# Kernel tuning notes

Measured on AMD Instinct MI355X. Metric: run time of the kernel, lower is better.

Reference implementation:

```python
import jax, jax.numpy as jnp
import numpy as np
from functools import partial

V, E, H, F = 32000, 256, 512, 256  # vocab, embed_dim, hidden_dim, num_filters
FS = (3, 4, 5)

def setup_inputs() -> dict:
    key = jax.random.key(0)
    ks = jax.random.split(key, 24)
    s = 0.02
    d = {}
    d["src"] = jax.random.randint(ks[0], (32, 512), 0, V)
    d["trg"] = jax.random.randint(ks[1], (32, 64), 0, V)
    # embeddings with padding_idx=0 zeroed
    d["enc_emb"] = (jax.random.normal(ks[2], (V, E)) * s).at[0].set(0.0)
    d["dec_emb"] = (jax.random.normal(ks[3], (V, E)) * s).at[0].set(0.0)
    # conv1d weights (out_channels=F, in_channels=E, kernel)
    d["conv_w3"] = jax.random.normal(ks[4], (F, E, 3)) * s
    d["conv_b3"] = jnp.zeros((F,))
    d["conv_w4"] = jax.random.normal(ks[5], (F, E, 4)) * s
    d["conv_b4"] = jnp.zeros((F,))
    d["conv_w5"] = jax.random.normal(ks[6], (F, E, 5)) * s
    d["conv_b5"] = jnp.zeros((F,))
    d["fc1_w"] = jax.random.normal(ks[7], (H, 3 * F)) * s
    d["fc1_b"] = jnp.zeros((H,))
    d["fc2_w"] = jax.random.normal(ks[8], (H, H)) * s
    d["fc2_b"] = jnp.zeros((H,))
    # 2-layer LSTM: layer1 input E+H, layer2 input H; gates order i,f,g,o
    d["w_ih1"] = jax.random.normal(ks[9], (4 * H, E + H)) * s
    d["w_hh1"] = jax.random.normal(ks[10], (4 * H, H)) * s
    d["b_ih1"] = jnp.zeros((4 * H,))
    d["b_hh1"] = jnp.zeros((4 * H,))
    d["w_ih2"] = jax.random.normal(ks[11], (4 * H, H)) * s
    d["w_hh2"] = jax.random.normal(ks[12], (4 * H, H)) * s
    d["b_ih2"] = jnp.zeros((4 * H,))
    d["b_hh2"] = jnp.zeros((4 * H,))
    d["out_w"] = jax.random.normal(ks[13], (V, H)) * s
    d["out_b"] = jnp.zeros((V,))
    return d

def _lstm_cell(x, h, c, w_ih, w_hh, b_ih, b_hh):
    gates = x @ w_ih.T + b_ih + h @ w_hh.T + b_hh  # (B, 4H)
    i, f, g, o = jnp.split(gates, 4, axis=-1)
    c_new = jax.nn.sigmoid(f) * c + jax.nn.sigmoid(i) * jnp.tanh(g)
    h_new = jax.nn.sigmoid(o) * jnp.tanh(c_new)
    return h_new, c_new

def _encoder(src, enc_emb, convs, fc1_w, fc1_b, fc2_w, fc2_b):
    x = enc_emb[src]                    # (B, S, E)
    x = jnp.transpose(x, (0, 2, 1))     # (B, E, S)
    pooled = []
    for w, b in convs:
        y = jax.lax.conv_general_dilated(
            x, w, window_strides=(1,), padding='VALID',
            dimension_numbers=('NCH', 'OIH', 'NCH'))  # (B, F, S-k+1)
        pooled.append(jnp.max(jax.nn.relu(y + b[None, :, None]), axis=2))
    cat = jnp.concatenate(pooled, axis=1)              # (B, 3F)
    h = jax.nn.relu(cat @ fc1_w.T + fc1_b)             # (B, H)
    return h @ fc2_w.T + fc2_b                         # (B, H)

def reference(src, trg, enc_emb, conv_w3, conv_b3, conv_w4, conv_b4,
              conv_w5, conv_b5, fc1_w, fc1_b, fc2_w, fc2_b, dec_emb,
              w_ih1, w_hh1, b_ih1, b_hh1, w_ih2, w_hh2, b_ih2, b_hh2,
              out_w, out_b):
    B, T = trg.shape
    enc_out = _encoder(src, enc_emb,
                       [(conv_w3, conv_b3), (conv_w4, conv_b4), (conv_w5, conv_b5)],
                       fc1_w, fc1_b, fc2_w, fc2_b)  # (B, H)

    def step(carry, tok):
        h1, c1, h2, c2 = carry
        x = jnp.concatenate([dec_emb[tok], enc_out], axis=1)  # (B, E+H)
        h1, c1 = _lstm_cell(x, h1, c1, w_ih1, w_hh1, b_ih1, b_hh1)
        h2, c2 = _lstm_cell(h1, h2, c2, w_ih2, w_hh2, b_ih2, b_hh2)
        logits = h2 @ out_w.T + out_b                          # (B, V)
        return (h1, c1, h2, c2), logits

    z = jnp.zeros((B, H), dtype=enc_out.dtype)
    tokens = trg[:, :-1].T  # teacher forcing (ratio=1.0): (T-1, B)
    _, logits = jax.lax.scan(step, (z, z, z, z), tokens)       # (T-1, B, V)
    logits = jnp.transpose(logits, (1, 0, 2))                  # (B, T-1, V)
    # outputs[:, 0] is left as zeros, matching the torch loop starting at t=1
    return jnp.concatenate([jnp.zeros((B, 1, logits.shape[-1]), logits.dtype), logits], axis=1)
```

## Files before the change

### kernel.cpp

```cpp
#include <hip/hip_runtime.h>
#include <math.h>
#include <stdint.h>

#define B_    32
#define E_    256
#define F_    256
#define H_    512
#define V_    32000
#define G4    2048

typedef unsigned short u16;
typedef unsigned long long u64;
typedef __attribute__((ext_vector_type(8))) short bf16x8;
typedef __attribute__((ext_vector_type(4))) float f32x4;

__device__ __forceinline__ float fsig(float x) {
  return __builtin_amdgcn_rcpf(1.f + __expf(-x));
}
__device__ __forceinline__ float ftanh(float x) {
  return 1.f - 2.f * __builtin_amdgcn_rcpf(1.f + __expf(2.f * x));
}

__device__ __forceinline__ u16 f2bf(float f) {
  uint32_t u = __float_as_uint(f);
  uint32_t r = (u + 0x7FFFu + ((u >> 16) & 1u)) >> 16;
  return (u16)r;
}
__device__ __forceinline__ uint32_t pack2(float a, float b) {
  return (uint32_t)f2bf(a) | ((uint32_t)f2bf(b) << 16);
}

#define GLOAD16(gp, lp) __builtin_amdgcn_global_load_lds( \
    (const __attribute__((address_space(1))) uint32_t*)(const void*)(gp), \
    (__attribute__((address_space(3))) uint32_t*)(void*)(lp), 16, 0, 0)

#define ALOAD(P) __hip_atomic_load((P), __ATOMIC_RELAXED, __HIP_MEMORY_SCOPE_AGENT)
#define ASTORE(P, V) __hip_atomic_store((P), (V), __ATOMIC_RELAXED, __HIP_MEMORY_SCOPE_AGENT)

__global__ void init_all(float* pooled, uint32_t* sent1, uint32_t* sent2,
                         u16* h1d, u16* h2a,
                         const float* bi1, const float* bh1,
                         const float* bi2, const float* bh2,
                         float* bs1, float* bs2, float* out) {
  int i = blockIdx.x * blockDim.x + threadIdx.x, st = gridDim.x * blockDim.x;
  for (int k = i; k < 24576; k += st) pooled[k] = 0.f;
  for (int k = i; k < 131072; k += st) {
    uint32_t v = (k < 2048 && (k & 15) == 0) ? 1u : 0u;
    sent1[k] = v; sent2[k] = v;
  }
  uint4 z = {0u, 0u, 0u, 0u};
  for (int k = i; k < 2048; k += st) { ((uint4*)h1d)[k] = z; ((uint4*)h2a)[k] = z; }
  for (int k = i; k < G4; k += st) { bs1[k] = bi1[k] + bh1[k]; bs2[k] = bi2[k] + bh2[k]; }
  for (int k = i; k < B_ * V_; k += st) {
    int b = k / V_, v = k - b * V_;
    out[(size_t)b * 64 * V_ + v] = 0.f;
  }
}

__global__ void cvt_all(const float* s0, u16* d0, const float* s1, u16* d1,
                        const float* s2, u16* d2, const float* s3, u16* d3,
                        const float* s4, u16* d4) {
  int i = blockIdx.x * blockDim.x + threadIdx.x, st = gridDim.x * blockDim.x;
  for (; i < 2637824; i += st) {
    int j = i; const float* s; u16* d;
    if (j < 2048000) { s = s0; d = d0; }
    else if ((j -= 2048000) < 196608) { s = s1; d = d1; }
    else if ((j -= 196608) < 131072) { s = s2; d = d2; }
    else if ((j -= 131072) < 131072) { s = s3; d = d3; }
    else { j -= 131072; s = s4; d = d4; }
    const float4* sp = (const float4*)s + 2 * (size_t)j;
    float4 a = sp[0], b = sp[1];
    uint4 u;
    u.x = pack2(a.x, a.y); u.y = pack2(a.z, a.w);
    u.z = pack2(b.x, b.y); u.w = pack2(b.z, b.w);
    *((uint4*)d + j) = u;
  }
}

__global__ void wtj_all(const float* w3, u16* t3, const float* w4, u16* t4,
                        const float* w5, u16* t5) {
  int i = blockIdx.x * blockDim.x + threadIdx.x, st = gridDim.x * blockDim.x;
  for (; i < 786432; i += st) {
    int j = i; const float* w; u16* wt; int kw;
    if (j < 196608) { w = w3; wt = t3; kw = 3; }
    else if ((j -= 196608) < 262144) { w = w4; wt = t4; kw = 4; }
    else { j -= 262144; w = w5; wt = t5; kw = 5; }
    int f = j / (kw * 256);
    int r = j - f * (kw * 256);
    int jj = r >> 8, e = r & 255;
    wt[j] = f2bf(w[(f * 256 + e) * kw + jj]);
  }
}

__global__ void build_x1(const int* __restrict__ trg, const float* __restrict__ demb,
                         const float* __restrict__ enco, u16* __restrict__ X1) {
  int r = blockIdx.x, tid = threadIdx.x;
  u16* row = X1 + (size_t)r * 768;
  if (r >= 2016) { row[tid] = 0; row[256 + tid] = 0; row[512 + tid] = 0; return; }
  int t = r >> 5, b = r & 31;
  int tok = trg[b * 64 + t];
  row[tid]       = f2bf(demb[(size_t)tok * E_ + tid]);
  row[256 + tid] = f2bf(enco[b * H_ + tid]);
  row[512 + tid] = f2bf(enco[b * H_ + 256 + tid]);
}

__global__ void gemm_small(const float* __restrict__ A, const float* __restrict__ W,
                           const float* __restrict__ bias, float* __restrict__ C,
                           int K, int N, int relu) {
  int nl = threadIdx.x & 7, b = threadIdx.x >> 3;
  int n = blockIdx.x * 8 + nl;
  const float* a = A + b * K;
  const float* w = W + (size_t)n * K;
  float acc = 0.f;
  for (int k = 0; k < K; k += 4) {
    float4 av = *reinterpret_cast<const float4*>(&a[k]);
    float4 wv = *reinterpret_cast<const float4*>(&w[k]);
    acc = fmaf(av.x, wv.x, acc); acc = fmaf(av.y, wv.y, acc);
    acc = fmaf(av.z, wv.z, acc); acc = fmaf(av.w, wv.w, acc);
  }
  acc += bias[n];
  if (relu) acc = fmaxf(acc, 0.f);
  C[b * N + n] = acc;
}

__global__ __launch_bounds__(256)
void gemm_mfma(const u16* __restrict__ A, const u16* __restrict__ Bw,
               const float* __restrict__ bias, float* __restrict__ C,
               int M, int N, int K) {
  __shared__ char smem[32768];
  const int tid = threadIdx.x;
  const int wid = tid >> 6, lane = tid & 63;
  const int hi = lane >> 4, lo = lane & 15;
  const int wr = wid >> 1, wc = wid & 1;
  const int m0 = blockIdx.x * 128, n0 = blockIdx.y * 128;
  const int NT = K >> 5;
  const int srow = lane >> 2, sc = lane & 3;

  f32x4 acc[4][4];
#pragma unroll
  for (int i = 0; i < 4; ++i)
#pragma unroll
    for (int j = 0; j < 4; ++j) acc[i][j] = (f32x4){0.f, 0.f, 0.f, 0.f};

  for (int t = -1; t < NT; ++t) {
    int ts = t + 1;
    if (ts < NT) {
      char* base = smem + (ts & 1) * 16384;
      int k0 = ts << 5;
#pragma unroll
      for (int q = 0; q < 2; ++q) {
        int row = (wid + q * 4) * 16 + srow;
        int gc = sc ^ (row & 3);
        const char* gp = (const char*)A + (((size_t)(m0 + row) * K + k0) << 1) + gc * 16;
        GLOAD16(gp, base + (wid + q * 4) * 1024);
      }
#pragma unroll
      for (int q = 0; q < 2; ++q) {
        int row = (wid + q * 4) * 16 + srow;
        int gc = sc ^ (row & 3);
        const char* gp = (const char*)Bw + (((size_t)(n0 + row) * K + k0) << 1) + gc * 16;
        GLOAD16(gp, base + 8192 + (wid + q * 4) * 1024);
      }
    }
    if (t >= 0) {
      char* base = smem + (t & 1) * 16384;
      bf16x8 af[4], bfr[4];
#pragma unroll
      for (int mi = 0; mi < 4; ++mi) {
        int row = wr * 64 + mi * 16 + lo;
        af[mi] = *(const bf16x8*)(base + row * 64 + ((hi ^ (row & 3)) << 4));
      }
#pragma unroll
      for (int ni = 0; ni < 4; ++ni) {
        int row = wc * 64 + ni * 16 + lo;
        bfr[ni] = *(const bf16x8*)(base + 8192 + row * 64 + ((hi ^ (row & 3)) << 4));
      }
#pragma unroll
      for (int mi = 0; mi < 4; ++mi)
#pragma unroll
        for (int ni = 0; ni < 4; ++ni)
          acc[mi][ni] = __builtin_amdgcn_mfma_f32_16x16x32_bf16(af[mi], bfr[ni], acc[mi][ni], 0, 0, 0);
    }
    __syncthreads();
  }

#pragma unroll
  for (int mi = 0; mi < 4; ++mi)
#pragma unroll
    for (int r = 0; r < 4; ++r) {
      int m = m0 + wr * 64 + mi * 16 + hi * 4 + r;
      if (m >= M) continue;
      size_t rowbase = (size_t)m * N;
#pragma unroll
      for (int ni = 0; ni < 4; ++ni) {
        int col = n0 + wc * 64 + ni * 16 + lo;
        C[rowbase + col] = acc[mi][ni][r] + bias[col];
      }
    }
}

__global__ __launch_bounds__(256)
void conv_mfma(const u16* __restrict__ wt3, const u16* __restrict__ wt4,
               const u16* __restrict__ wt5,
               const float* __restrict__ cb3, const float* __restrict__ cb4,
               const float* __restrict__ cb5,
               float* __restrict__ pooled,
               const int* __restrict__ srcTok, const float* __restrict__ emb) {
  const int z = blockIdx.z;
  const u16* Bw = (z == 0) ? wt3 : (z == 1) ? wt4 : wt5;
  const float* bias = (z == 0) ? cb3 : (z == 1) ? cb4 : cb5;
  const int K = 768 + 256 * z, kw = 3 + z, poolOff = 256 * z;

  __shared__ char smem[32768];
  const int tid = threadIdx.x;
  const int wid = tid >> 6, lane = tid & 63;
  const int hi = lane >> 4, lo = lane & 15;
  const int wr = wid >> 1, wc = wid & 1;
  const int m0 = blockIdx.x * 128, n0 = blockIdx.y * 128;
  const int NT = K >> 5;
  const int srow = lane >> 2, sc = lane & 3;

  f32x4 acc[4][4];
#pragma unroll
  for (int i = 0; i < 4; ++i)
#pragma unroll
    for (int j = 0; j < 4; ++j) acc[i][j] = (f32x4){0.f, 0.f, 0.f, 0.f};

  for (int t = -1; t < NT; ++t) {
    int ts = t + 1;
    if (ts < NT) {
      char* base = smem + (ts & 1) * 16384;
      int k0 = ts << 5;
      {
        int j = k0 >> 8, e0 = k0 & 255;
        int row = tid >> 1;
        int m = m0 + row;
        int s = m & 511, b = m >> 9;
        int sj = s + j;
        int tok = (sj < 512) ? srcTok[b * 512 + sj] : -1;
#pragma unroll
        for (int q = 0; q < 2; ++q) {
          int cg = (tid & 1) * 2 + q;
          uint4 u;
          if (tok >= 0) {
            const float* ep = emb + (size_t)tok * 256 + e0 + cg * 8;
            float4 f0 = *(const float4*)(ep);
            float4 f1 = *(const float4*)(ep + 4);
            u.x = pack2(f0.x, f0.y); u.y = pack2(f0.z, f0.w);
            u.z = pack2(f1.x, f1.y); u.w = pack2(f1.z, f1.w);
          } else u = (uint4){0, 0, 0, 0};
          int c = cg ^ (row & 3);
          *(uint4*)(base + row * 64 + c * 16) = u;
        }
      }
#pragma unroll
      for (int q = 0; q < 2; ++q) {
        int row = (wid + q * 4) * 16 + srow;
        int gc = sc ^ (row & 3);
        const char* gp = (const char*)Bw + (((size_t)(n0 + row) * K + k0) << 1) + gc * 16;
        GLOAD16(gp, base + 8192 + (wid + q * 4) * 1024);
      }
    }
    if (t >= 0) {
      char* base = smem + (t & 1) * 16384;
      bf16x8 af[4], bfr[4];
#pragma unroll
      for (int mi = 0; mi < 4; ++mi) {
        int row = wr * 64 + mi * 16 + lo;
        af[mi] = *(const bf16x8*)(base + row * 64 + ((hi ^ (row & 3)) << 4));
      }
#pragma unroll
      for (int ni = 0; ni < 4; ++ni) {
        int row = wc * 64 + ni * 16 + lo;
        bfr[ni] = *(const bf16x8*)(base + 8192 + row * 64 + ((hi ^ (row & 3)) << 4));
      }
#pragma unroll
      for (int mi = 0; mi < 4; ++mi)
#pragma unroll
        for (int ni = 0; ni < 4; ++ni)
          acc[mi][ni] = __builtin_amdgcn_mfma_f32_16x16x32_bf16(af[mi], bfr[ni], acc[mi][ni], 0, 0, 0);
    }
    __syncthreads();
  }

  int b = m0 >> 9;
  int slim = 512 - kw;
#pragma unroll
  for (int ni = 0; ni < 4; ++ni) {
    int col = n0 + wc * 64 + ni * 16 + lo;
    float bv = bias[col];
    float mx = 0.f;
#pragma unroll
    for (int mi = 0; mi < 4; ++mi)
#pragma unroll
      for (int r = 0; r < 4; ++r) {
        int m = m0 + wr * 64 + mi * 16 + hi * 4 + r;
        int s = m & 511;
        float v = acc[mi][ni][r] + bv;
        if (s <= slim && v > mx) mx = v;
      }
    atomicMax((int*)&pooled[b * 768 + poolOff + col], __float_as_int(mx));
  }
}

__global__ __launch_bounds__(256, 1)
void lstm_fused(const float* __restrict__ pre,
                const u16* __restrict__ whh1,
                const u16* __restrict__ wih2, const u16* __restrict__ whh2,
                const float* __restrict__ bs2,
                uint32_t* __restrict__ sent1, uint32_t* __restrict__ sent2,
                u16* __restrict__ h1d, u16* __restrict__ h2a,
                const u16* __restrict__ outw_bf, const float* __restrict__ outb,
                float* __restrict__ out) {
  __shared__ char smem[74752];
  const int tid = threadIdx.x;
  const int wid = tid >> 6, lane = tid & 63, hi = lane >> 4, lo = lane & 15;
  const int hrow = tid >> 3, k8 = tid & 7;
  const int pb = hrow, pj0 = k8 * 2;

#define WAVE_DRAIN() asm volatile("s_waitcnt vmcnt(0)" ::: "memory")
#define POLL1(P) while (ALOAD(P) == 0u) __builtin_amdgcn_s_sleep(1);
#define POLL2(P, Q) for (;;) { uint32_t x_ = ALOAD(P), y_ = ALOAD(Q); \
                               if (x_ & y_) break; __builtin_amdgcn_s_sleep(1); }
#define POLL2S(P, Q) for (;;) { uint32_t x_ = ALOAD(P), y_ = ALOAD(Q); \
                                if (x_ & y_) break; __builtin_amdgcn_s_sleep(16); }

  if (blockIdx.x < 32) {
    const int bi = blockIdx.x;
    u16* hlds = (u16*)smem;
    float* glds = (float*)(smem + 33280);

    bf16x8 wreg[16];
    const u16* wp = whh1 + (((size_t)(wid * 512 + bi * 16 + lo)) << 9) + hi * 8;
#pragma unroll
    for (int ks = 0; ks < 16; ++ks) wreg[ks] = *(const bf16x8*)(wp + ks * 32);

    float creg0 = 0.f, creg1 = 0.f;

    for (int t = 0; t < 63; ++t) {
      const float* pr = pre + (((size_t)(t * 32 + pb)) << 11) + bi * 16 + pj0;
      float pi0 = pr[0], pf0 = pr[512], pg0 = pr[1024], po0 = pr[1536];
      float pi1 = pr[1], pf1 = pr[513], pg1 = pr[1025], po1 = pr[1537];

      const u64* hp = (const u64*)(h1d + ((size_t)t * 32 + hrow) * 512);
      f32x4 acc0 = (f32x4){0.f,0.f,0.f,0.f}, acc1 = (f32x4){0.f,0.f,0.f,0.f};

      POLL1(sent1 + (size_t)t * 2048 + lane * 16)
      {
        u64 v[8];
#pragma unroll
        for (int g = 0; g < 4; ++g) {
          int c = k8 + 8 * g;
          v[2*g]   = ALOAD(hp + 2 * c);
          v[2*g+1] = ALOAD(hp + 2 * c + 1);
        }
#pragma unroll
        for (int g = 0; g < 4; ++g) {
          int c = k8 + 8 * g;
          u64 w2[2] = { v[2*g], v[2*g+1] };
          *(uint4*)(hlds + hrow * 520 + c * 8) = *(const uint4*)w2;
        }
      }
      __syncthreads();
#pragma unroll
      for (int ks = 0; ks < 8; ++ks) {
        int cg = (ks * 4 + hi) * 8;
        bf16x8 a0 = *(const bf16x8*)(hlds + lo * 520 + cg);
        bf16x8 a1 = *(const bf16x8*)(hlds + (16 + lo) * 520 + cg);
        acc0 = __builtin_amdgcn_mfma_f32_16x16x32_bf16(a0, wreg[ks], acc0, 0, 0, 0);
        acc1 = __builtin_amdgcn_mfma_f32_16x16x32_bf16(a1, wreg[ks], acc1, 0, 0, 0);
      }
      POLL1(sent1 + (size_t)t * 2048 + (64 + lane) * 16)
      {
        u64 v[8];
#pragma unroll
        for (int g = 0; g < 4; ++g) {
          int c = 32 + k8 + 8 * g;
          v[2*g]   = ALOAD(hp + 2 * c);
          v[2*g+1] = ALOAD(hp + 2 * c + 1);
        }
#pragma unroll
        for (int g = 0; g < 4; ++g) {
          int c = 32 + k8 + 8 * g;
          u64 w2[2] = { v[2*g], v[2*g+1] };
          *(uint4*)(hlds + hrow * 520 + c * 8) = *(const uint4*)w2;
        }
      }
      __syncthreads();
#pragma unroll
      for (int ks = 8; ks < 16; ++ks) {
        int cg = (ks * 4 + hi) * 8;
        bf16x8 a0 = *(const bf16x8*)(hlds + lo * 520 + cg);
        bf16x8 a1 = *(const bf16x8*)(hlds + (16 + lo) * 520 + cg);
        acc0 = __builtin_amdgcn_mfma_f32_16x16x32_bf16(a0, wreg[ks], acc0, 0, 0, 0);
        acc1 = __builtin_amdgcn_mfma_f32_16x16x32_bf16(a1, wreg[ks], acc1, 0, 0, 0);
      }
#pragma unroll
      for (int r = 0; r < 4; ++r) {
        glds[wid * 544 + (hi * 4 + r) * 17 + lo] = acc0[r];
        glds[wid * 544 + (16 + hi * 4 + r) * 17 + lo] = acc1[r];
      }
      __syncthreads();

      float iv0 = glds[0*544 + pb*17 + pj0]   + pi0, fv0 = glds[1*544 + pb*17 + pj0]   + pf0;
      float gv0 = glds[2*544 + pb*17 + pj0]   + pg0, ov0 = glds[3*544 + pb*17 + pj0]   + po0;
      float iv1 = glds[0*544 + pb*17 + pj0+1] + pi1, fv1 = glds[1*544 + pb*17 + pj0+1] + pf1;
      float gv1 = glds[2*544 + pb*17 + pj0+1] + pg1, ov1 = glds[3*544 + pb*17 + pj0+1] + po1;
      float cn0 = fsig(fv0) * creg0 + fsig(iv0) * ftanh(gv0);
      float hn0 = fsig(ov0) * ftanh(cn0);
      float cn1 = fsig(fv1) * creg1 + fsig(iv1) * ftanh(gv1);
      float hn1 = fsig(ov1) * ftanh(cn1);
      creg0 = cn0; creg1 = cn1;
      ASTORE((uint32_t*)(h1d + ((size_t)(t + 1) * 32 + pb) * 512 + bi * 16 + pj0),
             pack2(hn0, hn1));
      WAVE_DRAIN();
      if (lane == 0)
        ASTORE(sent1 + (size_t)(t + 1) * 2048 + (bi * 4 + wid) * 16, 1u);
    }
  } else if (blockIdx.x < 64) {
    const int bi2 = blockIdx.x - 32;
    u16* alds = (u16*)smem;
    float* glds = (float*)(smem + 66048);

    bf16x8 wreg[32];
    {
      const u16* wa = wih2 + (((size_t)(wid * 512 + bi2 * 16 + lo)) << 9) + hi * 8;
      const u16* wb = whh2 + (((size_t)(wid * 512 + bi2 * 16 + lo)) << 9) + hi * 8;
#pragma unroll
      for (int ks = 0; ks < 16; ++ks) {
        wreg[ks]      = *(const bf16x8*)(wa + ks * 32);
        wreg[16 + ks] = *(const bf16x8*)(wb + ks * 32);
      }
    }
    float bsv0 = bs2[0 * 512 + bi2 * 16 + pj0], bsv0b = bs2[0 * 512 + bi2 * 16 + pj0 + 1];
    float bsv1 = bs2[1 * 512 + bi2 * 16 + pj0], bsv1b = bs2[1 * 512 + bi2 * 16 + pj0 + 1];
    float bsv2 = bs2[2 * 512 + bi2 * 16 + pj0], bsv2b = bs2[2 * 512 + bi2 * 16 + pj0 + 1];
    float bsv3 = bs2[3 * 512 + bi2 * 16 + pj0], bsv3b = bs2[3 * 512 + bi2 * 16 + pj0 + 1];

    float creg0 = 0.f, creg1 = 0.f;

    for (int t = 0; t < 63; ++t) {
      f32x4 acc0 = (f32x4){0.f,0.f,0.f,0.f}, acc1 = (f32x4){0.f,0.f,0.f,0.f};

      POLL2(sent1 + (size_t)(t + 1) * 2048 + lane * 16,
            sent1 + (size_t)(t + 1) * 2048 + (64 + lane) * 16)
      {
        const u64* hp1 = (const u64*)(h1d + ((size_t)(t + 1) * 32 + hrow) * 512);
        u64 v[16];
#pragma unroll
        for (int g = 0; g < 8; ++g) {
          int c = k8 + 8 * g;
          v[2*g]   = ALOAD(hp1 + 2 * c);
          v[2*g+1] = ALOAD(hp1 + 2 * c + 1);
        }
#pragma unroll
        for (int g = 0; g < 8; ++g) {
          int c = k8 + 8 * g;
          u64 w2[2] = { v[2*g], v[2*g+1] };
          *(uint4*)(alds + hrow * 1032 + c * 8) = *(const uint4*)w2;
        }
      }
      __syncthreads();
#pragma unroll
      for (int ks = 0; ks < 16; ++ks) {
        int cg = (ks * 4 + hi) * 8;
        bf16x8 a0 = *(const bf16x8*)(alds + lo * 1032 + cg);
        bf16x8 a1 = *(const bf16x8*)(alds + (16 + lo) * 1032 + cg);
        acc0 = __builtin_amdgcn_mfma_f32_16x16x32_bf16(a0, wreg[ks], acc0, 0, 0, 0);
        acc1 = __builtin_amdgcn_mfma_f32_16x16x32_bf16(a1, wreg[ks], acc1, 0, 0, 0);
      }
      POLL2(sent2 + (size_t)t * 2048 + lane * 16,
            sent2 + (size_t)t * 2048 + (64 + lane) * 16)
      {
        const u64* hp2 = (const u64*)(h2a + ((size_t)t * 32 + hrow) * 512);
        u64 v[16];
#pragma unroll
        for (int g = 0; g < 8; ++g) {
          int c = k8 + 8 * g;
          v[2*g]   = ALOAD(hp2 + 2 * c);
          v[2*g+1] = ALOAD(hp2 + 2 * c + 1);
        }
#pragma unroll
        for (int g = 0; g < 8; ++g) {
          int c = 64 + k8 + 8 * g;
          u64 w2[2] = { v[2*g], v[2*g+1] };
          *(uint4*)(alds + hrow * 1032 + c * 8) = *(const uint4*)w2;
        }
      }
      __syncthreads();
#pragma unroll
      for (int ks = 0; ks < 16; ++ks) {
        int cg = (64 + ks * 4 + hi) * 8;
        bf16x8 a0 = *(const bf16x8*)(alds + lo * 1032 + cg);
        bf16x8 a1 = *(const bf16x8*)(alds + (16 + lo) * 1032 + cg);
        acc0 = __builtin_amdgcn_mfma_f32_16x16x32_bf16(a0, wreg[16 + ks], acc0, 0, 0, 0);
        acc1 = __builtin_amdgcn_mfma_f32_16x16x32_bf16(a1, wreg[16 + ks], acc1, 0, 0, 0);
      }
#pragma unroll
      for (int r = 0; r < 4; ++r) {
        glds[wid * 544 + (hi * 4 + r) * 17 + lo] = acc0[r];
        glds[wid * 544 + (16 + hi * 4 + r) * 17 + lo] = acc1[r];
      }
      __syncthreads();

      float gi0 = glds[0*544 + pb*17 + pj0]   + bsv0,  gf0 = glds[1*544 + pb*17 + pj0]   + bsv1;
      float gg0 = glds[2*544 + pb*17 + pj0]   + bsv2,  go0 = glds[3*544 + pb*17 + pj0]   + bsv3;
      float gi1 = glds[0*544 + pb*17 + pj0+1] + bsv0b, gf1 = glds[1*544 + pb*17 + pj0+1] + bsv1b;
      float gg1 = glds[2*544 + pb*17 + pj0+1] + bsv2b, go1 = glds[3*544 + pb*17 + pj0+1] + bsv3b;
      float cn0 = fsig(gf0) * creg0 + fsig(gi0) * ftanh(gg0);
      float hn0 = fsig(go0) * ftanh(cn0);
      float cn1 = fsig(gf1) * creg1 + fsig(gi1) * ftanh(gg1);
      float hn1 = fsig(go1) * ftanh(cn1);
      creg0 = cn0; creg1 = cn1;
      ASTORE((uint32_t*)(h2a + ((size_t)(t + 1) * 32 + pb) * 512 + bi2 * 16 + pj0),
             pack2(hn0, hn1));
      WAVE_DRAIN();
      if (lane == 0)
        ASTORE(sent2 + (size_t)(t + 1) * 2048 + (bi2 * 4 + wid) * 16, 1u);
    }
  } else {
    const int bid2 = blockIdx.x - 64;
    const int wr = wid >> 1, wc = wid & 1;
    const int srow = lane >> 2, sc = lane & 3;
    const u16* A = h2a + 16384;

    for (int w = bid2; w < 16 * 250; w += 160) {
      int rt = w / 250, ct = w - rt * 250;
      int tf = rt * 4 + 4; if (tf > 63) tf = 63;
      if (wid == 0)
        POLL2S(sent2 + (size_t)tf * 2048 + lane * 16,
               sent2 + (size_t)tf * 2048 + (64 + lane) * 16)
      __syncthreads();

      const int m0 = rt * 128, n0 = ct * 128;
      f32x4 acc[4][4];
#pragma unroll
      for (int i = 0; i < 4; ++i)
#pragma unroll
        for (int j = 0; j < 4; ++j) acc[i][j] = (f32x4){0.f, 0.f, 0.f, 0.f};

      for (int t = -1; t < 16; ++t) {
        int ts = t + 1;
        if (ts < 16) {
          char* base = smem + (ts & 1) * 16384;
          int k0 = ts << 5;
#pragma unroll
          for (int q = 0; q < 2; ++q) {
            int row = (wid + q * 4) * 16 + srow;
            int gc = sc ^ (row & 3);
            const char* gp = (const char*)A + (((size_t)(m0 + row) * 512 + k0) << 1) + gc * 16;
            GLOAD16(gp, base + (wid + q * 4) * 1024);
          }
#pragma unroll
          for (int q = 0; q < 2; ++q) {
            int row = (wid + q * 4) * 16 + srow;
            int gc = sc ^ (row & 3);
            const char* gp = (const char*)outw_bf + (((size_t)(n0 + row) * 512 + k0) << 1) + gc * 16;
            GLOAD16(gp, base + 8192 + (wid + q * 4) * 1024);
          }
        }
        if (t >= 0) {
          char* base = smem + (t & 1) * 16384;
          bf16x8 af[4], bfr[4];
#pragma unroll
          for (int mi = 0; mi < 4; ++mi) {
            int row = wr * 64 + mi * 16 + lo;
            af[mi] = *(const bf16x8*)(base + row * 64 + ((hi ^ (row & 3)) << 4));
          }
#pragma unroll
          for (int ni = 0; ni < 4; ++ni) {
            int row = wc * 64 + ni * 16 + lo;
            bfr[ni] = *(const bf16x8*)(base + 8192 + row * 64 + ((hi ^ (row & 3)) << 4));
          }
#pragma unroll
          for (int mi = 0; mi < 4; ++mi)
#pragma unroll
            for (int ni = 0; ni < 4; ++ni)
              acc[mi][ni] = __builtin_amdgcn_mfma_f32_16x16x32_bf16(af[mi], bfr[ni], acc[mi][ni], 0, 0, 0);
        }
        __syncthreads();
      }

#pragma unroll
      for (int mi = 0; mi < 4; ++mi)
#pragma unroll
        for (int r = 0; r < 4; ++r) {
          int m = m0 + wr * 64 + mi * 16 + hi * 4 + r;
          if (m >= 2016) continue;
          int t2 = m >> 5, b = m & 31;
          size_t rowbase = ((size_t)b * 64 + t2 + 1) * (size_t)V_;
#pragma unroll
          for (int ni = 0; ni < 4; ++ni) {
            int col = n0 + wc * 64 + ni * 16 + lo;
            out[rowbase + col] = acc[mi][ni][r] + outb[col];
          }
        }
    }
  }
#undef POLL1
#undef POLL2
#undef POLL2S
#undef WAVE_DRAIN
}

extern "C" void kernel_launch(void* const* d_in, const int* in_sizes, int n_in,
                              void* d_out, int out_size, void* d_ws, size_t ws_size,
                              hipStream_t stream) {
  const int*   src  = (const int*)  d_in[0];
  const int*   trg  = (const int*)  d_in[1];
  const float* eemb = (const float*)d_in[2];
  const float* demb = (const float*)d_in[3];
  const float* cw3  = (const float*)d_in[4];
  const float* cb3  = (const float*)d_in[5];
  const float* cw4  = (const float*)d_in[6];
  const float* cb4  = (const float*)d_in[7];
  const float* cw5  = (const float*)d_in[8];
  const float* cb5  = (const float*)d_in[9];
  const float* fc1w = (const float*)d_in[10];
  const float* fc1b = (const float*)d_in[11];
  const float* fc2w = (const float*)d_in[12];
  const float* fc2b = (const float*)d_in[13];
  const float* wih1 = (const float*)d_in[14];
  const float* whh1 = (const float*)d_in[15];
  const float* bih1 = (const float*)d_in[16];
  const float* bhh1 = (const float*)d_in[17];
  const float* wih2 = (const float*)d_in[18];
  const float* whh2 = (const float*)d_in[19];
  const float* bih2 = (const float*)d_in[20];
  const float* bhh2 = (const float*)d_in[21];
  const float* outw = (const float*)d_in[22];
  const float* outb = (const float*)d_in[23];
  float* out = (float*)d_out;

  uint32_t* sent1 = (uint32_t*)d_ws;
  uint32_t* sent2 = sent1 + 131072;
  u16* h1d      = (u16*)(sent2 + 131072);
  u16* h2a      = h1d + 1048576;
  float* pooled = (float*)(h2a + 1048576);
  float* ench   = pooled + 24576;
  float* enco   = ench + 16384;
  float* bs1    = enco + 16384;
  float* bs2    = bs1 + 2048;
  float* pre    = bs2 + 2048;
  u16* outw_bf  = (u16*)(pre + 4128768);
  u16* wih1_bf  = outw_bf + 16384000;
  u16* wih2_bf  = wih1_bf + 1572864;
  u16* whh1_bf  = wih2_bf + 1048576;
  u16* whh2_bf  = whh1_bf + 1048576;
  u16* wtj3     = whh2_bf + 1048576;
  u16* wtj4     = wtj3 + 196608;
  u16* wtj5     = wtj4 + 262144;
  u16* X1       = wtj5 + 327680;

  init_all<<<512, 256, 0, stream>>>(pooled, sent1, sent2, h1d, h2a,
                                    bih1, bhh1, bih2, bhh2, bs1, bs2, out);
  cvt_all<<<2048, 256, 0, stream>>>(outw, outw_bf, wih1, wih1_bf, wih2, wih2_bf,
                                    whh1, whh1_bf, whh2, whh2_bf);
  wtj_all<<<512, 256, 0, stream>>>(cw3, wtj3, cw4, wtj4, cw5, wtj5);

  conv_mfma<<<dim3(128, 2, 3), 256, 0, stream>>>(wtj3, wtj4, wtj5, cb3, cb4, cb5,
                                                 pooled, src, eemb);
  gemm_small<<<64, 256, 0, stream>>>(pooled, fc1w, fc1b, ench, 768, 512, 1);
  gemm_small<<<64, 256, 0, stream>>>(ench, fc2w, fc2b, enco, 512, 512, 0);

  build_x1<<<2048, 256, 0, stream>>>(trg, demb, enco, X1);
  gemm_mfma<<<dim3(16, 16), 256, 0, stream>>>(X1, wih1_bf, bs1, pre, 2016, 2048, 768);
  lstm_fused<<<224, 256, 0, stream>>>(pre, whh1_bf, wih2_bf, whh2_bf, bs2,
                                      sent1, sent2, h1d, h2a, outw_bf, outb, out);
}
```

Baseline: 471.3 us.

## Fuse layer-1 input GEMM into persistent LSTM kernel with per-row-tile counters

Removes the separate build_x1 and gemm_mfma launches. The 160 idle output-projection blocks of lstm_fused now compute the layer-1 input projection, gathering embeddings and encoder output directly into shared memory. They publish each 128-row tile through an atomic counter that the recurrent blocks poll every four timesteps, so the input GEMM overlaps with the LSTM recurrence. Output writes also switch to nontemporal stores. The cost is extra polling and synchronisation, and a risk of stalls if the GEMM blocks fall behind the recurrence.

```diff
diff --git a/kernel.cpp b/kernel.cpp
--- a/kernel.cpp
+++ b/kernel.cpp
@@ -38,7 +38,7 @@
 #define ASTORE(P, V) __hip_atomic_store((P), (V), __ATOMIC_RELAXED, __HIP_MEMORY_SCOPE_AGENT)
 
 __global__ void init_all(float* pooled, uint32_t* sent1, uint32_t* sent2,
-                         u16* h1d, u16* h2a,
+                         uint32_t* cnt1, u16* h1d, u16* h2a,
                          const float* bi1, const float* bh1,
                          const float* bi2, const float* bh2,
                          float* bs1, float* bs2, float* out) {
@@ -48,12 +48,13 @@
     uint32_t v = (k < 2048 && (k & 15) == 0) ? 1u : 0u;
     sent1[k] = v; sent2[k] = v;
   }
+  for (int k = i; k < 256; k += st) cnt1[k] = 0u;
   uint4 z = {0u, 0u, 0u, 0u};
   for (int k = i; k < 2048; k += st) { ((uint4*)h1d)[k] = z; ((uint4*)h2a)[k] = z; }
   for (int k = i; k < G4; k += st) { bs1[k] = bi1[k] + bh1[k]; bs2[k] = bi2[k] + bh2[k]; }
   for (int k = i; k < B_ * V_; k += st) {
     int b = k / V_, v = k - b * V_;
-    out[(size_t)b * 64 * V_ + v] = 0.f;
+    __builtin_nontemporal_store(0.f, &out[(size_t)b * 64 * V_ + v]);
   }
 }
 
@@ -92,18 +93,6 @@
   }
 }
 
-__global__ void build_x1(const int* __restrict__ trg, const float* __restrict__ demb,
-                         const float* __restrict__ enco, u16* __restrict__ X1) {
-  int r = blockIdx.x, tid = threadIdx.x;
-  u16* row = X1 + (size_t)r * 768;
-  if (r >= 2016) { row[tid] = 0; row[256 + tid] = 0; row[512 + tid] = 0; return; }
-  int t = r >> 5, b = r & 31;
-  int tok = trg[b * 64 + t];
-  row[tid]       = f2bf(demb[(size_t)tok * E_ + tid]);
-  row[256 + tid] = f2bf(enco[b * H_ + tid]);
-  row[512 + tid] = f2bf(enco[b * H_ + 256 + tid]);
-}
-
 __global__ void gemm_small(const float* __restrict__ A, const float* __restrict__ W,
                            const float* __restrict__ bias, float* __restrict__ C,
                            int K, int N, int relu) {
@@ -124,82 +113,6 @@
 }
 
 __global__ __launch_bounds__(256)
-void gemm_mfma(const u16* __restrict__ A, const u16* __restrict__ Bw,
-               const float* __restrict__ bias, float* __restrict__ C,
-               int M, int N, int K) {
-  __shared__ char smem[32768];
-  const int tid = threadIdx.x;
-  const int wid = tid >> 6, lane = tid & 63;
-  const int hi = lane >> 4, lo = lane & 15;
-  const int wr = wid >> 1, wc = wid & 1;
-  const int m0 = blockIdx.x * 128, n0 = blockIdx.y * 128;
-  const int NT = K >> 5;
-  const int srow = lane >> 2, sc = lane & 3;
-
-  f32x4 acc[4][4];
-#pragma unroll
-  for (int i = 0; i < 4; ++i)
-#pragma unroll
-    for (int j = 0; j < 4; ++j) acc[i][j] = (f32x4){0.f, 0.f, 0.f, 0.f};
-
-  for (int t = -1; t < NT; ++t) {
-    int ts = t + 1;
-    if (ts < NT) {
-      char* base = smem + (ts & 1) * 16384;
-      int k0 = ts << 5;
-#pragma unroll
-      for (int q = 0; q < 2; ++q) {
-        int row = (wid + q * 4) * 16 + srow;
-        int gc = sc ^ (row & 3);
-        const char* gp = (const char*)A + (((size_t)(m0 + row) * K + k0) << 1) + gc * 16;
-        GLOAD16(gp, base + (wid + q * 4) * 1024);
-      }
-#pragma unroll
-      for (int q = 0; q < 2; ++q) {
-        int row = (wid + q * 4) * 16 + srow;
-        int gc = sc ^ (row & 3);
-        const char* gp = (const char*)Bw + (((size_t)(n0 + row) * K + k0) << 1) + gc * 16;
-        GLOAD16(gp, base + 8192 + (wid + q * 4) * 1024);
-      }
-    }
-    if (t >= 0) {
-      char* base = smem + (t & 1) * 16384;
-      bf16x8 af[4], bfr[4];
-#pragma unroll
-      for (int mi = 0; mi < 4; ++mi) {
-        int row = wr * 64 + mi * 16 + lo;
-        af[mi] = *(const bf16x8*)(base + row * 64 + ((hi ^ (row & 3)) << 4));
-      }
-#pragma unroll
-      for (int ni = 0; ni < 4; ++ni) {
-        int row = wc * 64 + ni * 16 + lo;
-        bfr[ni] = *(const bf16x8*)(base + 8192 + row * 64 + ((hi ^ (row & 3)) << 4));
-      }
-#pragma unroll
-      for (int mi = 0; mi < 4; ++mi)
-#pragma unroll
-        for (int ni = 0; ni < 4; ++ni)
-          acc[mi][ni] = __builtin_amdgcn_mfma_f32_16x16x32_bf16(af[mi], bfr[ni], acc[mi][ni], 0, 0, 0);
-    }
-    __syncthreads();
-  }
-
-#pragma unroll
-  for (int mi = 0; mi < 4; ++mi)
-#pragma unroll
-    for (int r = 0; r < 4; ++r) {
-      int m = m0 + wr * 64 + mi * 16 + hi * 4 + r;
-      if (m >= M) continue;
-      size_t rowbase = (size_t)m * N;
-#pragma unroll
-      for (int ni = 0; ni < 4; ++ni) {
-        int col = n0 + wc * 64 + ni * 16 + lo;
-        C[rowbase + col] = acc[mi][ni][r] + bias[col];
-      }
-    }
-}
-
-__global__ __launch_bounds__(256)
 void conv_mfma(const u16* __restrict__ wt3, const u16* __restrict__ wt4,
                const u16* __restrict__ wt5,
                const float* __restrict__ cb3, const float* __restrict__ cb4,
@@ -304,14 +217,18 @@
 }
 
 __global__ __launch_bounds__(256, 1)
-void lstm_fused(const float* __restrict__ pre,
+void lstm_fused(float* __restrict__ pre,
                 const u16* __restrict__ whh1,
                 const u16* __restrict__ wih2, const u16* __restrict__ whh2,
                 const float* __restrict__ bs2,
                 uint32_t* __restrict__ sent1, uint32_t* __restrict__ sent2,
+                uint32_t* __restrict__ cnt1,
                 u16* __restrict__ h1d, u16* __restrict__ h2a,
                 const u16* __restrict__ outw_bf, const float* __restrict__ outb,
-                float* __restrict__ out) {
+                float* __restrict__ out,
+                const int* __restrict__ trg, const float* __restrict__ demb,
+                const float* __restrict__ enco,
+                const u16* __restrict__ wih1_bf, const float* __restrict__ bs1) {
   __shared__ char smem[74752];
   const int tid = threadIdx.x;
   const int wid = tid >> 6, lane = tid & 63, hi = lane >> 4, lo = lane & 15;
@@ -338,6 +255,11 @@
     float creg0 = 0.f, creg1 = 0.f;
 
     for (int t = 0; t < 63; ++t) {
+      if ((t & 3) == 0) {
+        if (tid == 0)
+          while (ALOAD(cnt1 + (t >> 2) * 16) < 16u) __builtin_amdgcn_s_sleep(8);
+        __syncthreads();
+      }
       const float* pr = pre + (((size_t)(t * 32 + pb)) << 11) + bi * 16 + pj0;
       float pi0 = pr[0], pf0 = pr[512], pg0 = pr[1024], po0 = pr[1536];
       float pi1 = pr[1], pf1 = pr[513], pg1 = pr[1025], po1 = pr[1537];
@@ -522,6 +444,93 @@
     const int bid2 = blockIdx.x - 64;
     const int wr = wid >> 1, wc = wid & 1;
     const int srow = lane >> 2, sc = lane & 3;
+
+    for (int w = bid2; w < 256; w += 160) {
+      int rt = w >> 4, ct = w & 15;
+      const int m0 = rt * 128, n0 = ct * 128;
+      f32x4 acc[4][4];
+#pragma unroll
+      for (int i = 0; i < 4; ++i)
+#pragma unroll
+        for (int j = 0; j < 4; ++j) acc[i][j] = (f32x4){0.f, 0.f, 0.f, 0.f};
+
+      for (int t = -1; t < 24; ++t) {
+        int ts = t + 1;
+        if (ts < 24) {
+          char* base = smem + (ts & 1) * 16384;
+          int k0 = ts << 5;
+          {
+            int row = tid >> 1;
+            int m = m0 + row;
+            int tt = m >> 5, b = m & 31;
+            int ok = (m < 2016);
+            int tok = ok ? trg[b * 64 + tt] : 0;
+#pragma unroll
+            for (int q = 0; q < 2; ++q) {
+              int cg = (tid & 1) * 2 + q;
+              int k = k0 + cg * 8;
+              uint4 u;
+              if (ok) {
+                const float* ep = (k < 256) ? (demb + (size_t)tok * 256 + k)
+                                            : (enco + (size_t)b * 512 + (k - 256));
+                float4 f0 = *(const float4*)(ep);
+                float4 f1 = *(const float4*)(ep + 4);
+                u.x = pack2(f0.x, f0.y); u.y = pack2(f0.z, f0.w);
+                u.z = pack2(f1.x, f1.y); u.w = pack2(f1.z, f1.w);
+              } else u = (uint4){0, 0, 0, 0};
+              int c = cg ^ (row & 3);
+              *(uint4*)(base + row * 64 + c * 16) = u;
+            }
+          }
+#pragma unroll
+          for (int q = 0; q < 2; ++q) {
+            int row = (wid + q * 4) * 16 + srow;
+            int gc = sc ^ (row & 3);
+            const char* gp = (const char*)wih1_bf + (((size_t)(n0 + row) * 768 + k0) << 1) + gc * 16;
+            GLOAD16(gp, base + 8192 + (wid + q * 4) * 1024);
+          }
+        }
+        if (t >= 0) {
+          char* base = smem + (t & 1) * 16384;
+          bf16x8 af[4], bfr[4];
+#pragma unroll
+          for (int mi = 0; mi < 4; ++mi) {
+            int row = wr * 64 + mi * 16 + lo;
+            af[mi] = *(const bf16x8*)(base + row * 64 + ((hi ^ (row & 3)) << 4));
+          }
+#pragma unroll
+          for (int ni = 0; ni < 4; ++ni) {
+            int row = wc * 64 + ni * 16 + lo;
+            bfr[ni] = *(const bf16x8*)(base + 8192 + row * 64 + ((hi ^ (row & 3)) << 4));
+          }
+#pragma unroll
+          for (int mi = 0; mi < 4; ++mi)
+#pragma unroll
+            for (int ni = 0; ni < 4; ++ni)
+              acc[mi][ni] = __builtin_amdgcn_mfma_f32_16x16x32_bf16(af[mi], bfr[ni], acc[mi][ni], 0, 0, 0);
+        }
+        __syncthreads();
+      }
+#pragma unroll
+      for (int mi = 0; mi < 4; ++mi)
+#pragma unroll
+        for (int r = 0; r < 4; ++r) {
+          int m = m0 + wr * 64 + mi * 16 + hi * 4 + r;
+          if (m >= 2016) continue;
+#pragma unroll
+          for (int ni = 0; ni < 4; ++ni) {
+            int col = n0 + wc * 64 + ni * 16 + lo;
+            ASTORE((uint32_t*)(pre + (size_t)m * 2048 + col),
+                   __float_as_uint(acc[mi][ni][r] + bs1[col]));
+          }
+        }
+      WAVE_DRAIN();
+      __syncthreads();
+      if (tid == 0)
+        __hip_atomic_fetch_add(cnt1 + rt * 16, 1u, __ATOMIC_RELAXED, __HIP_MEMORY_SCOPE_AGENT);
+      __syncthreads();
+    }
+
     const u16* A = h2a + 16384;
 
     for (int w = bid2; w < 16 * 250; w += 160) {
@@ -592,7 +601,7 @@
 #pragma unroll
           for (int ni = 0; ni < 4; ++ni) {
             int col = n0 + wc * 64 + ni * 16 + lo;
-            out[rowbase + col] = acc[mi][ni][r] + outb[col];
+            __builtin_nontemporal_store(acc[mi][ni][r] + outb[col], &out[rowbase + col]);
           }
         }
     }
@@ -634,7 +643,8 @@
 
   uint32_t* sent1 = (uint32_t*)d_ws;
   uint32_t* sent2 = sent1 + 131072;
-  u16* h1d      = (u16*)(sent2 + 131072);
+  uint32_t* cnt1  = sent2 + 131072;
+  u16* h1d      = (u16*)(cnt1 + 256);
   u16* h2a      = h1d + 1048576;
   float* pooled = (float*)(h2a + 1048576);
   float* ench   = pooled + 24576;
@@ -650,9 +660,8 @@
   u16* wtj3     = whh2_bf + 1048576;
   u16* wtj4     = wtj3 + 196608;
   u16* wtj5     = wtj4 + 262144;
-  u16* X1       = wtj5 + 327680;
-
-  init_all<<<512, 256, 0, stream>>>(pooled, sent1, sent2, h1d, h2a,
+
+  init_all<<<512, 256, 0, stream>>>(pooled, sent1, sent2, cnt1, h1d, h2a,
                                     bih1, bhh1, bih2, bhh2, bs1, bs2, out);
   cvt_all<<<2048, 256, 0, stream>>>(outw, outw_bf, wih1, wih1_bf, wih2, wih2_bf,
                                     whh1, whh1_bf, whh2, whh2_bf);
@@ -663,8 +672,8 @@
   gemm_small<<<64, 256, 0, stream>>>(pooled, fc1w, fc1b, ench, 768, 512, 1);
   gemm_small<<<64, 256, 0, stream>>>(ench, fc2w, fc2b, enco, 512, 512, 0);
 
-  build_x1<<<2048, 256, 0, stream>>>(trg, demb, enco, X1);
-  gemm_mfma<<<dim3(16, 16), 256, 0, stream>>>(X1, wih1_bf, bs1, pre, 2016, 2048, 768);
   lstm_fused<<<224, 256, 0, stream>>>(pre, whh1_bf, wih2_bf, whh2_bf, bs2,
-                                      sent1, sent2, h1d, h2a, outw_bf, outb, out);
-}
+                                      sent1, sent2, cnt1, h1d, h2a,
+                                      outw_bf, outb, out,
+                                      trg, demb, enco, wih1_bf, bs1);
+}
```

Result: no change. 467.3 us (-0.9%).
